# Optimization experiments

Measured on AMD Instinct MI355X. Metric: run time of the kernel, lower is better.

## Reference

```python
import jax, jax.numpy as jnp
import numpy as np

B, T, N, D = 4, 24, 325, 512


def setup_inputs() -> dict:
    key = jax.random.key(0)
    ks = jax.random.split(key, 8)
    s = 1.0 / np.sqrt(D)
    return {
        "X": jax.random.normal(ks[0], (B, T, N, D), jnp.float32),
        "Q": jax.random.normal(ks[1], (B, T, N, D), jnp.float32),
        "K": jax.random.normal(ks[2], (B, T, N, D), jnp.float32),
        "V": jax.random.normal(ks[3], (B, T, N, D), jnp.float32),
        "W_head": jax.random.normal(ks[4], (3, D, D), jnp.float32) * s,
        "bias": jax.random.normal(ks[5], (3, D), jnp.float32) * 0.02,
        "W_out": jax.random.normal(ks[6], (D, D), jnp.float32) * s,
        "ln_gamma": jnp.ones((D,), jnp.float32),
        "ln_beta": jnp.zeros((D,), jnp.float32),
        "n_head": 8,
    }


def reference(X, Q, K, V, W_head, bias, W_out, ln_gamma, ln_beta, n_head):
    b, t, n, d = X.shape
    d_k = d // n_head  # num_per_head

    def proj(inp, W, bvec):
        y = jnp.einsum('btnd,de->btne', inp, W) + bvec
        # torch: view(b,T,N,d_k,n_head).permute(-1,0,1,2,3) -> (h,b,t,n,d_k)
        y = y.reshape(b, t, n, d_k, n_head)
        return jnp.transpose(y, (4, 0, 1, 2, 3))

    q = proj(Q, W_head[0], bias[0])
    k = proj(K, W_head[1], bias[1])
    v = proj(V, W_head[2], bias[2])

    scores = jnp.einsum('hbtnd,hbtmd->hbtnm', q, k) / jnp.sqrt(jnp.asarray(d_k, X.dtype))
    attn = jax.nn.softmax(scores, axis=-1)
    o = jnp.einsum('hbtnm,hbtmd->hbtnd', attn, v)
    # inverse of the head split: (h,b,t,n,d_k) -> (b,t,n,d_k,h) -> (b,t,n,d)
    o = jnp.transpose(o, (1, 2, 3, 4, 0)).reshape(b, t, n, d)

    out = jnp.einsum('btnd,de->btne', o, W_out) + X  # out-proj + residual
    mu = jnp.mean(out, axis=-1, keepdims=True)
    var = jnp.mean(jnp.square(out - mu), axis=-1, keepdims=True)
    out = (out - mu) * jax.lax.rsqrt(var + 1e-5) * ln_gamma + ln_beta
    return out
```

## Files before the change

### kernel.cpp

```cpp
#include <hip/hip_runtime.h>
#include <hip/hip_bf16.h>
#include <stdint.h>

#define BB 4
#define TT 24
#define NN 325
#define DD 512
#define NH 8
#define DKH 64
#define MROWS (BB*TT*NN)
#define BTC (BB*TT)

typedef __attribute__((ext_vector_type(4))) float f32x4;
typedef __attribute__((ext_vector_type(8))) short s16x8;
typedef __attribute__((ext_vector_type(4))) unsigned int u32x4;
typedef __attribute__((ext_vector_type(2))) unsigned int u32x2;

__device__ __forceinline__ unsigned short f2bf(float f) {
    union { float f; unsigned int u; } x; x.f = f;
    unsigned int u = x.u;
    u += 0x7fffu + ((u >> 16) & 1u);
    return (unsigned short)(u >> 16);
}
__device__ __forceinline__ unsigned int cvt2(float a, float b) {
    unsigned int r;
    asm("v_cvt_pk_bf16_f32 %0, %1, %2" : "=v"(r) : "v"(a), "v"(b));
    return r;
}
__device__ __forceinline__ unsigned short bf1(float a) {
    return (unsigned short)cvt2(a, a);
}
__device__ __forceinline__ float bf2f(unsigned int u16) {
    union { float f; unsigned int u; } x; x.u = u16 << 16; return x.f;
}

__device__ __forceinline__ void gload16(const void* g, void* l) {
    __builtin_amdgcn_global_load_lds((const __attribute__((address_space(1))) void*)g,
                                     (__attribute__((address_space(3))) void*)l, 16, 0, 0);
}

#define MEMFENCE asm volatile("" ::: "memory")

__global__ void prep_kernel(const float* __restrict__ Wh, const float* __restrict__ bias,
                            const float* __restrict__ Wo,
                            unsigned short* __restrict__ WtH, unsigned short* __restrict__ WtO,
                            float* __restrict__ biasp)
{
    int idx = blockIdx.x * 256 + threadIdx.x;
    if (idx < 3*512*512) {
        int i = idx >> 18; int rem = idx & 262143;
        int cp = rem >> 9; int e = rem & 511;
        int c = ((cp & 63) << 3) | (cp >> 6);
        WtH[idx] = f2bf(Wh[(i << 18) + (e << 9) + c]);
        return;
    }
    int idx2 = idx - 3*512*512;
    if (idx2 >= 0 && idx2 < 512*512) {
        int c = idx2 >> 9; int ep = idx2 & 511;
        int row = ((ep & 63) << 3) | (ep >> 6);
        WtO[idx2] = f2bf(Wo[(row << 9) + c]);
        return;
    }
    int idx3 = idx2 - 512*512;
    if (idx3 >= 0 && idx3 < 3*512) {
        int i = idx3 >> 9; int cp = idx3 & 511;
        int c = ((cp & 63) << 3) | (cp >> 6);
        biasp[idx3] = bias[(i << 9) + c];
    }
}

__global__ __launch_bounds__(256) void projf_gemm3(
    const float* __restrict__ A0, const float* __restrict__ A1, const float* __restrict__ A2,
    const unsigned short* __restrict__ Wt, const float* __restrict__ biasp,
    unsigned short* __restrict__ Y0, unsigned short* __restrict__ Y1, unsigned short* __restrict__ Y2)
{
    __shared__ __align__(16) unsigned short Sh[4*128*64];

    int orig = blockIdx.x;
    int wg = (orig & 7) * 366 + (orig >> 3);
    int z = wg / 976; int rem = wg - z * 976;
    int mtile = rem >> 2; int ntile = rem & 3;

    const float* Ap = (z == 0) ? A0 : ((z == 1) ? A1 : A2);
    unsigned short* Y = (z == 0) ? Y0 : ((z == 1) ? Y1 : Y2);
    const unsigned short* Btn = Wt + z * 512 * 512 + ntile * 128 * 512;
    const float* bias = biasp + z * 512;

    int t = threadIdx.x;
    int wid = t >> 6, lane = t & 63;
    int wm = wid >> 1, wn = wid & 1;
    int lm = lane & 15, lg = lane >> 4;

    long mbase = (long)mtile * 128;

    int tr = t >> 4, tc = t & 15;
    long aoffg[8];
    int awr[8];
    #pragma unroll
    for (int i = 0; i < 8; ++i) {
        int rl = i * 16 + tr;
        long rg = mbase + rl; if (rg >= MROWS) rg = MROWS - 1;
        aoffg[i] = rg * 512 + tc * 4;
        awr[i] = rl * 16 + (((tc >> 1) ^ (rl & 7)) << 1) + (tc & 1);
    }
    int boff[4];
    #pragma unroll
    for (int r = 0; r < 4; ++r) {
        int G = ((r * 4 + wid) << 6) + lane;
        int row = G >> 3;
        int slot = (G & 7) ^ (row & 7);
        boff[r] = row * 512 + slot * 8;
    }

    f32x4 acc[4][4] = {};
    f32x4 ar[2][8];

#define LOADA(kk, S) { const int k0 = (kk) * 64;                               \
    _Pragma("unroll") for (int i = 0; i < 8; ++i)                              \
        ar[S][i] = *(const f32x4*)(Ap + aoffg[i] + k0); }
#define STAGEB(kk, b) { unsigned short* Bs_ = Sh + (b) * 16384 + 8192;         \
    const int k0 = (kk) * 64;                                                  \
    _Pragma("unroll") for (int r = 0; r < 4; ++r)                              \
        gload16(Btn + boff[r] + k0, &Bs_[(r * 4 + wid) << 9]); }
#define DSWA(S, b) { u32x2* dst_ = (u32x2*)(Sh + (b) * 16384);                 \
    _Pragma("unroll") for (int i = 0; i < 8; ++i) {                            \
        u32x2 w_; w_[0] = cvt2(ar[S][i][0], ar[S][i][1]);                      \
        w_[1] = cvt2(ar[S][i][2], ar[S][i][3]); dst_[awr[i]] = w_; } }

    LOADA(0, 0); MEMFENCE;
    STAGEB(0, 0); MEMFENCE;
    asm volatile("s_waitcnt vmcnt(4)" ::: "memory");
    DSWA(0, 0);
    LOADA(1, 1); MEMFENCE;
    STAGEB(1, 1); MEMFENCE;

    #pragma unroll
    for (int kk = 0; kk < 8; ++kk) {
        const int b = kk & 1;
        if (kk < 7) asm volatile("s_waitcnt vmcnt(12)" ::: "memory");
        else        asm volatile("s_waitcnt vmcnt(0)"  ::: "memory");
        asm volatile("s_waitcnt lgkmcnt(0)" ::: "memory");
        __builtin_amdgcn_s_barrier();

        if (kk <= 5) { LOADA(kk + 2, b); MEMFENCE; }

        const unsigned short* As = Sh + b * 16384;
        const unsigned short* Bs = As + 8192;
        #pragma unroll
        for (int ks = 0; ks < 2; ++ks) {
            s16x8 afr[4], bfr[4];
            #pragma unroll
            for (int mf = 0; mf < 4; ++mf) {
                int row = wm * 64 + mf * 16 + lm;
                afr[mf] = ((const s16x8*)As)[row * 8 + ((ks * 4 + lg) ^ (row & 7))];
            }
            #pragma unroll
            for (int nf = 0; nf < 4; ++nf) {
                int row = wn * 64 + nf * 16 + lm;
                bfr[nf] = ((const s16x8*)Bs)[row * 8 + ((ks * 4 + lg) ^ (row & 7))];
            }
            #pragma unroll
            for (int mf = 0; mf < 4; ++mf)
                #pragma unroll
                for (int nf = 0; nf < 4; ++nf)
                    acc[mf][nf] = __builtin_amdgcn_mfma_f32_16x16x32_bf16(afr[mf], bfr[nf], acc[mf][nf], 0, 0, 0);
        }
        MEMFENCE;
        __builtin_amdgcn_s_barrier();
        if (kk <= 5) { STAGEB(kk + 2, b); MEMFENCE; }
        if (kk <= 6) {
            if (kk <= 5) asm volatile("s_waitcnt vmcnt(16)" ::: "memory");
            else         asm volatile("s_waitcnt vmcnt(4)"  ::: "memory");
            DSWA((kk + 1) & 1, b ^ 1);
        }
    }
#undef LOADA
#undef STAGEB
#undef DSWA

    __syncthreads();
    #pragma unroll
    for (int nf = 0; nf < 4; ++nf) {
        int col = wn * 64 + nf * 16 + lm;
        float bv = bias[ntile * 128 + col];
        #pragma unroll
        for (int mf = 0; mf < 4; ++mf) {
            #pragma unroll
            for (int j = 0; j < 4; ++j) {
                int row = wm * 64 + mf * 16 + lg * 4 + j;
                Sh[row * 128 + (col ^ ((row & 12) << 2))] = bf1(acc[mf][nf][j] + bv);
            }
        }
    }
    __syncthreads();
    #pragma unroll
    for (int it = 0; it < 8; ++it) {
        int row = it * 16 + (t >> 4);
        int c8 = (t & 15) * 8;
        u32x4 v = *(const u32x4*)&Sh[row * 128 + (c8 ^ ((row & 12) << 2))];
        long grow = mbase + row;
        if (grow < MROWS)
            *(u32x4*)&Y[grow * 512 + ntile * 128 + c8] = v;
    }
}

__global__ __launch_bounds__(256) void out_gemm(
    const unsigned short* __restrict__ A, const unsigned short* __restrict__ Bt,
    const float* __restrict__ X, unsigned short* __restrict__ Out)
{
    __shared__ __align__(16) unsigned short Sh[4*128*64];

    int orig = blockIdx.x;
    int wg = (orig & 7) * 122 + (orig >> 3);
    int mtile = wg >> 2; int ntile = wg & 3;

    int t = threadIdx.x;
    int wid = t >> 6, lane = t & 63;
    int wm = wid >> 1, wn = wid & 1;
    int lm = lane & 15, lg = lane >> 4;

    long mbase = (long)mtile * 128;
    const unsigned short* Abase = A + mbase * 512;
    const unsigned short* Btn = Bt + ntile * 128 * 512;

    int aoff[4], boff[4];
    #pragma unroll
    for (int r = 0; r < 4; ++r) {
        int G = ((r * 4 + wid) << 6) + lane;
        int row = G >> 3;
        int slot = (G & 7) ^ (row & 7);
        int rowc = row;
        if (mbase + row > MROWS - 1) rowc = (int)(MROWS - 1 - mbase);
        aoff[r] = rowc * 512 + slot * 8;
        boff[r] = row * 512 + slot * 8;
    }

    f32x4 acc[4][4] = {};

    auto STAGE = [&](int kk, int b) {
        unsigned short* As = Sh + b * 16384;
        unsigned short* Bs = As + 8192;
        const int k0 = kk * 64;
        #pragma unroll
        for (int r = 0; r < 4; ++r)
            gload16(Abase + aoff[r] + k0, &As[(r * 4 + wid) << 9]);
        #pragma unroll
        for (int r = 0; r < 4; ++r)
            gload16(Btn + boff[r] + k0, &Bs[(r * 4 + wid) << 9]);
    };

    STAGE(0, 0);
    STAGE(1, 1);

    #pragma unroll
    for (int kk = 0; kk < 8; ++kk) {
        const int b = kk & 1;
        if (kk < 7) asm volatile("s_waitcnt vmcnt(8)" ::: "memory");
        else        asm volatile("s_waitcnt vmcnt(0)" ::: "memory");
        __builtin_amdgcn_s_barrier();

        const unsigned short* As = Sh + b * 16384;
        const unsigned short* Bs = As + 8192;
        #pragma unroll
        for (int ks = 0; ks < 2; ++ks) {
            s16x8 afr[4], bfr[4];
            #pragma unroll
            for (int mf = 0; mf < 4; ++mf) {
                int row = wm * 64 + mf * 16 + lm;
                afr[mf] = ((const s16x8*)As)[row * 8 + ((ks * 4 + lg) ^ (row & 7))];
            }
            #pragma unroll
            for (int nf = 0; nf < 4; ++nf) {
                int row = wn * 64 + nf * 16 + lm;
                bfr[nf] = ((const s16x8*)Bs)[row * 8 + ((ks * 4 + lg) ^ (row & 7))];
            }
            #pragma unroll
            for (int mf = 0; mf < 4; ++mf)
                #pragma unroll
                for (int nf = 0; nf < 4; ++nf)
                    acc[mf][nf] = __builtin_amdgcn_mfma_f32_16x16x32_bf16(afr[mf], bfr[nf], acc[mf][nf], 0, 0, 0);
        }
        MEMFENCE;
        __builtin_amdgcn_s_barrier();
        if (kk + 2 < 8) STAGE(kk + 2, b);
    }

    __syncthreads();
    #pragma unroll
    for (int nf = 0; nf < 4; ++nf) {
        int col = wn * 64 + nf * 16 + lm;
        #pragma unroll
        for (int mf = 0; mf < 4; ++mf) {
            #pragma unroll
            for (int j = 0; j < 4; ++j) {
                int row = wm * 64 + mf * 16 + lg * 4 + j;
                Sh[row * 128 + (col ^ ((row & 12) << 2))] = bf1(acc[mf][nf][j]);
            }
        }
    }
    __syncthreads();
    #pragma unroll
    for (int it = 0; it < 8; ++it) {
        int row = it * 16 + (t >> 4);
        int c8 = (t & 15) * 8;
        u32x4 v = *(const u32x4*)&Sh[row * 128 + (c8 ^ ((row & 12) << 2))];
        long grow = mbase + row;
        if (grow < MROWS) {
            long gidx = grow * 512 + ntile * 128 + c8;
            const float* xp = X + gidx;
            f32x4 x0 = *(const f32x4*)xp, x1 = *(const f32x4*)(xp + 4);
            float xx[8] = {x0[0], x0[1], x0[2], x0[3], x1[0], x1[1], x1[2], x1[3]};
            u32x4 o;
            #pragma unroll
            for (int q = 0; q < 4; ++q) {
                float lo = bf2f(v[q] & 0xffffu) + xx[2 * q];
                float hi = bf2f(v[q] >> 16)     + xx[2 * q + 1];
                o[q] = cvt2(lo, hi);
            }
            *(u32x4*)&Out[gidx] = o;
        }
    }
}

#define SCALE2 0.18033688f

__global__ __launch_bounds__(256) void attn_kernel(
    const unsigned short* __restrict__ Qw, const unsigned short* __restrict__ Kw,
    const unsigned short* __restrict__ Vw, unsigned short* __restrict__ Ow)
{
    __shared__ __align__(16) unsigned short Qs[128*64];
    __shared__ __align__(16) unsigned short Ks[64*64];
    __shared__ __align__(16) unsigned short Vts[64*64];
    __shared__ __align__(16) unsigned short Ps[4][16*64];

    int bid = blockIdx.x;
    int x = bid & 7, s = bid >> 3;
    int qc = s % 3;
    int gi = s / 3;
    int g  = x + 8 * gi;
    int h  = g & 7, bt = g >> 3;

    int t = threadIdx.x;
    int wid = t >> 6, lane = t & 63, lm = lane & 15, lg = lane >> 4;

    long rowbase = (long)bt * NN;
    int colbase = h * 64;
    int q0 = qc * 128;

    {
        int i = t >> 1, half = t & 1;
        int rowc = q0 + i; if (rowc > NN - 1) rowc = NN - 1;
        const u32x4* src = (const u32x4*)(Qw + (rowbase + rowc) * 512 + colbase);
        u32x4* dst = (u32x4*)Qs;
        #pragma unroll
        for (int ss = 0; ss < 4; ++ss) {
            int slot = half * 4 + ss;
            dst[i * 8 + (slot ^ (i & 7))] = src[slot];
        }
    }
    __syncthreads();
    s16x8 aq[2][2];
    #pragma unroll
    for (int qs = 0; qs < 2; ++qs) {
        int row = qs * 64 + wid * 16 + lm;
        aq[qs][0] = ((const s16x8*)Qs)[row * 8 + ((0 + lg) ^ (row & 7))];
        aq[qs][1] = ((const s16x8*)Qs)[row * 8 + ((4 + lg) ^ (row & 7))];
    }

    f32x4 oacc[2][4] = {};
    float lsum[2][4] = {};

    for (int tile = 0; tile < 6; ++tile) {
        const int kv0 = tile * 64;
        __syncthreads();
        #pragma unroll
        for (int r = 0; r < 2; ++r) {
            int G = r * 256 + t;
            int row = G >> 3;
            int slot = (G & 7) ^ (row & 7);
            int rowg = kv0 + row; if (rowg > NN - 1) rowg = NN - 1;
            gload16(Kw + (rowbase + rowg) * 512 + colbase + slot * 8, &Ks[G * 8]);
        }
        {
            int i = t >> 2, quarter = t & 3;
            int rowc = kv0 + i; if (rowc > NN - 1) rowc = NN - 1;
            const u32x4* src = (const u32x4*)(Vw + (rowbase + rowc) * 512 + colbase + quarter * 16);
            unsigned short vb[16] __attribute__((aligned(16)));
            *((u32x4*)vb) = src[0];
            *((u32x4*)(vb + 8)) = src[1];
            #pragma unroll
            for (int e = 0; e < 16; ++e) {
                int dk = quarter * 16 + e;
                int sv = (dk & 7) ^ ((dk >> 3) & 7);
                Vts[dk * 64 + (i ^ (sv << 3))] = vb[e];
            }
        }
        asm volatile("s_waitcnt vmcnt(0)" ::: "memory");
        __syncthreads();

        const bool tail = (tile == 5);
        #pragma unroll
        for (int qs = 0; qs < 2; ++qs) {
            f32x4 sacc[4] = {};
            #pragma unroll
            for (int ks = 0; ks < 2; ++ks) {
                #pragma unroll
                for (int nf = 0; nf < 4; ++nf) {
                    int row = nf * 16 + lm;
                    s16x8 bk = ((const s16x8*)Ks)[row * 8 + ((ks*4 + lg) ^ (row & 7))];
                    sacc[nf] = __builtin_amdgcn_mfma_f32_16x16x32_bf16(aq[qs][ks], bk, sacc[nf], 0, 0, 0);
                }
            }
            #pragma unroll
            for (int nf = 0; nf < 4; ++nf) {
                bool valid = !tail || (kv0 + nf * 16 + lm < NN);
                #pragma unroll
                for (int j = 0; j < 4; ++j) {
                    float pv = valid ? exp2f(sacc[nf][j] * SCALE2) : 0.f;
                    lsum[qs][j] += pv;
                    int r = lg * 4 + j;
                    int col = nf * 16 + lm;
                    Ps[wid][r * 64 + (col ^ (((r >> 1) & 7) << 3))] = bf1(pv);
                }
            }
            #pragma unroll
            for (int ks = 0; ks < 2; ++ks) {
                s16x8 ap = ((const s16x8*)Ps[wid])[lm * 8 + ((ks*4 + lg) ^ ((lm >> 1) & 7))];
                #pragma unroll
                for (int df = 0; df < 4; ++df) {
                    int vrow = df * 16 + lm;
                    int sv = (vrow & 7) ^ ((vrow >> 3) & 7);
                    s16x8 bv = ((const s16x8*)Vts)[vrow * 8 + ((ks*4 + lg) ^ sv)];
                    oacc[qs][df] = __builtin_amdgcn_mfma_f32_16x16x32_bf16(ap, bv, oacc[qs][df], 0, 0, 0);
                }
            }
        }
    }

    #pragma unroll
    for (int qs = 0; qs < 2; ++qs) {
        float inv[4];
        #pragma unroll
        for (int j = 0; j < 4; ++j) {
            float v = lsum[qs][j];
            v += __shfl_xor(v, 1, 16);
            v += __shfl_xor(v, 2, 16);
            v += __shfl_xor(v, 4, 16);
            v += __shfl_xor(v, 8, 16);
            inv[j] = __builtin_amdgcn_rcpf(v);
        }
        #pragma unroll
        for (int df = 0; df < 4; ++df) {
            int dk = df * 16 + lm;
            #pragma unroll
            for (int j = 0; j < 4; ++j) {
                int rloc = q0 + qs * 64 + wid * 16 + lg * 4 + j;
                if (rloc < NN)
                    Ow[(rowbase + rloc) * 512 + colbase + dk] = bf1(oacc[qs][df][j] * inv[j]);
            }
        }
    }
}

__global__ __launch_bounds__(256) void ln_kernel(
    const unsigned short* __restrict__ T, const float* __restrict__ gamma,
    const float* __restrict__ beta, float* __restrict__ Outp)
{
    int wid = threadIdx.x >> 6, lane = threadIdx.x & 63;
    long row = (long)blockIdx.x * 4 + wid;
    s16x8 h = ((const s16x8*)(T + row * 512))[lane];
    float v[8];
    #pragma unroll
    for (int j = 0; j < 8; ++j) v[j] = bf2f((unsigned int)(unsigned short)h[j]);
    float s = 0.f, sq = 0.f;
    #pragma unroll
    for (int j = 0; j < 8; ++j) { s += v[j]; sq += v[j] * v[j]; }
    #pragma unroll
    for (int m = 1; m < 64; m <<= 1) {
        s  += __shfl_xor(s, m);
        sq += __shfl_xor(sq, m);
    }
    float mean = s * (1.f / 512.f);
    float var = sq * (1.f / 512.f) - mean * mean;
    float rstd = rsqrtf(var + 1e-5f);
    const float4* g = (const float4*)gamma;
    const float4* b = (const float4*)beta;
    float4 g0 = g[lane * 2], g1 = g[lane * 2 + 1];
    float4 b0 = b[lane * 2], b1 = b[lane * 2 + 1];
    float4 o0, o1;
    o0.x = (v[0] - mean) * rstd * g0.x + b0.x;
    o0.y = (v[1] - mean) * rstd * g0.y + b0.y;
    o0.z = (v[2] - mean) * rstd * g0.z + b0.z;
    o0.w = (v[3] - mean) * rstd * g0.w + b0.w;
    o1.x = (v[4] - mean) * rstd * g1.x + b1.x;
    o1.y = (v[5] - mean) * rstd * g1.y + b1.y;
    o1.z = (v[6] - mean) * rstd * g1.z + b1.z;
    o1.w = (v[7] - mean) * rstd * g1.w + b1.w;
    float4* dst = (float4*)(Outp + row * 512);
    dst[lane * 2]     = o0;
    dst[lane * 2 + 1] = o1;
}

extern "C" void kernel_launch(void* const* d_in, const int* in_sizes, int n_in,
                              void* d_out, int out_size, void* d_ws, size_t ws_size,
                              hipStream_t stream)
{
    const float* X  = (const float*)d_in[0];
    const float* Q  = (const float*)d_in[1];
    const float* K  = (const float*)d_in[2];
    const float* V  = (const float*)d_in[3];
    const float* Wh = (const float*)d_in[4];
    const float* bi = (const float*)d_in[5];
    const float* Wo = (const float*)d_in[6];
    const float* gamma = (const float*)d_in[7];
    const float* beta  = (const float*)d_in[8];

    char* ws = (char*)d_ws;
    const size_t msz = (size_t)MROWS * 512 * 2;
    unsigned short* q_ws = (unsigned short*)(ws);
    unsigned short* k_ws = (unsigned short*)(ws + msz);
    unsigned short* v_ws = (unsigned short*)(ws + 2 * msz);
    unsigned short* o_ws = (unsigned short*)(ws + 3 * msz);
    unsigned short* WtH  = (unsigned short*)(ws + 4 * msz);
    unsigned short* WtO  = WtH + 3 * 512 * 512;
    float* biasp         = (float*)(ws + 4 * msz + (size_t)4*512*512*2);
    unsigned short* tmpb = q_ws;

    prep_kernel<<<4102, 256, 0, stream>>>(Wh, bi, Wo, WtH, WtO, biasp);

    projf_gemm3<<<2928, 256, 0, stream>>>(Q, K, V, WtH, biasp, q_ws, k_ws, v_ws);

    attn_kernel<<<2304, 256, 0, stream>>>(q_ws, k_ws, v_ws, o_ws);

    out_gemm<<<976, 256, 0, stream>>>(o_ws, WtO, X, tmpb);

    ln_kernel<<<7800, 256, 0, stream>>>(tmpb, gamma, beta, (float*)d_out);
}
```

Before: 233.1 us.

## Double-buffer K tiles and prefetch V into registers in attention kernel

After: 263.8 us. 1.13x slower.

```diff
diff --git a/kernel.cpp b/kernel.cpp
--- a/kernel.cpp
+++ b/kernel.cpp
@@ -328,10 +328,10 @@
     const unsigned short* __restrict__ Qw, const unsigned short* __restrict__ Kw,
     const unsigned short* __restrict__ Vw, unsigned short* __restrict__ Ow)
 {
-    __shared__ __align__(16) unsigned short Qs[128*64];
-    __shared__ __align__(16) unsigned short Ks[64*64];
-    __shared__ __align__(16) unsigned short Vts[64*64];
-    __shared__ __align__(16) unsigned short Ps[4][16*64];
+    __shared__ __align__(16) unsigned short Sh[16384];
+    unsigned short* Qs  = Sh;
+    unsigned short* Vts = Sh + 8192;
+    unsigned short* Psb = Sh + 12288;
 
     int bid = blockIdx.x;
     int x = bid & 7, s = bid >> 3;
@@ -366,38 +366,72 @@
         aq[qs][0] = ((const s16x8*)Qs)[row * 8 + ((0 + lg) ^ (row & 7))];
         aq[qs][1] = ((const s16x8*)Qs)[row * 8 + ((4 + lg) ^ (row & 7))];
     }
+    __syncthreads();
 
     f32x4 oacc[2][4] = {};
     float lsum[2][4] = {};
 
+    int vi = t >> 2, vq = t & 3;
+    u32x4 vr[2][2];
+
+    {
+        int rowc = vi; if (rowc > NN - 1) rowc = NN - 1;
+        const u32x4* src = (const u32x4*)(Vw + (rowbase + rowc) * 512 + colbase + vq * 16);
+        vr[0][0] = src[0]; vr[0][1] = src[1];
+    }
+    MEMFENCE;
+    #pragma unroll
+    for (int r = 0; r < 2; ++r) {
+        int G = r * 256 + t;
+        int row = G >> 3;
+        int slot = (G & 7) ^ (row & 7);
+        int rowg = row; if (rowg > NN - 1) rowg = NN - 1;
+        gload16(Kw + (rowbase + rowg) * 512 + colbase + slot * 8, &Sh[G * 8]);
+    }
+    MEMFENCE;
+
+    #pragma unroll
     for (int tile = 0; tile < 6; ++tile) {
+        const int pb = tile & 1;
+        unsigned short* Ks = Sh + pb * 4096;
+
+        asm volatile("s_waitcnt vmcnt(2)" ::: "memory");
+        {
+            unsigned short vb[16] __attribute__((aligned(16)));
+            *((u32x4*)vb) = vr[pb][0];
+            *((u32x4*)(vb + 8)) = vr[pb][1];
+            #pragma unroll
+            for (int e = 0; e < 16; ++e) {
+                int dk = vq * 16 + e;
+                int sv = (dk & 7) ^ ((dk >> 3) & 7);
+                Vts[dk * 64 + (vi ^ (sv << 3))] = vb[e];
+            }
+        }
+        asm volatile("s_waitcnt vmcnt(0)" ::: "memory");
+        asm volatile("s_waitcnt lgkmcnt(0)" ::: "memory");
+        __builtin_amdgcn_s_barrier();
+
+        if (tile < 5) {
+            const int kv1 = (tile + 1) * 64;
+            {
+                int rowc = kv1 + vi; if (rowc > NN - 1) rowc = NN - 1;
+                const u32x4* src = (const u32x4*)(Vw + (rowbase + rowc) * 512 + colbase + vq * 16);
+                vr[pb ^ 1][0] = src[0]; vr[pb ^ 1][1] = src[1];
+            }
+            MEMFENCE;
+            unsigned short* Kn = Sh + (pb ^ 1) * 4096;
+            #pragma unroll
+            for (int r = 0; r < 2; ++r) {
+                int G = r * 256 + t;
+                int row = G >> 3;
+                int slot = (G & 7) ^ (row & 7);
+                int rowg = kv1 + row; if (rowg > NN - 1) rowg = NN - 1;
+                gload16(Kw + (rowbase + rowg) * 512 + colbase + slot * 8, &Kn[G * 8]);
+            }
+            MEMFENCE;
+        }
+
         const int kv0 = tile * 64;
-        __syncthreads();
-        #pragma unroll
-        for (int r = 0; r < 2; ++r) {
-            int G = r * 256 + t;
-            int row = G >> 3;
-            int slot = (G & 7) ^ (row & 7);
-            int rowg = kv0 + row; if (rowg > NN - 1) rowg = NN - 1;
-            gload16(Kw + (rowbase + rowg) * 512 + colbase + slot * 8, &Ks[G * 8]);
-        }
-        {
-            int i = t >> 2, quarter = t & 3;
-            int rowc = kv0 + i; if (rowc > NN - 1) rowc = NN - 1;
-            const u32x4* src = (const u32x4*)(Vw + (rowbase + rowc) * 512 + colbase + quarter * 16);
-            unsigned short vb[16] __attribute__((aligned(16)));
-            *((u32x4*)vb) = src[0];
-            *((u32x4*)(vb + 8)) = src[1];
-            #pragma unroll
-            for (int e = 0; e < 16; ++e) {
-                int dk = quarter * 16 + e;
-                int sv = (dk & 7) ^ ((dk >> 3) & 7);
-                Vts[dk * 64 + (i ^ (sv << 3))] = vb[e];
-            }
-        }
-        asm volatile("s_waitcnt vmcnt(0)" ::: "memory");
-        __syncthreads();
-
         const bool tail = (tile == 5);
         #pragma unroll
         for (int qs = 0; qs < 2; ++qs) {
@@ -411,6 +445,7 @@
                     sacc[nf] = __builtin_amdgcn_mfma_f32_16x16x32_bf16(aq[qs][ks], bk, sacc[nf], 0, 0, 0);
                 }
             }
+            unsigned short* Ps = Psb + wid * 1024;
             #pragma unroll
             for (int nf = 0; nf < 4; ++nf) {
                 bool valid = !tail || (kv0 + nf * 16 + lm < NN);
@@ -420,12 +455,12 @@
                     lsum[qs][j] += pv;
                     int r = lg * 4 + j;
                     int col = nf * 16 + lm;
-                    Ps[wid][r * 64 + (col ^ (((r >> 1) & 7) << 3))] = bf1(pv);
+                    Ps[r * 64 + (col ^ (((r >> 1) & 7) << 3))] = bf1(pv);
                 }
             }
             #pragma unroll
             for (int ks = 0; ks < 2; ++ks) {
-                s16x8 ap = ((const s16x8*)Ps[wid])[lm * 8 + ((ks*4 + lg) ^ ((lm >> 1) & 7))];
+                s16x8 ap = ((const s16x8*)Ps)[lm * 8 + ((ks*4 + lg) ^ ((lm >> 1) & 7))];
                 #pragma unroll
                 for (int df = 0; df < 4; ++df) {
                     int vrow = df * 16 + lm;
@@ -435,6 +470,8 @@
                 }
             }
         }
+        MEMFENCE;
+        __builtin_amdgcn_s_barrier();
     }
 
     #pragma unroll
```
